# Kernel optimization log

Hardware: AMD Instinct MI355X
Metric: run time of the kernel (lower is better)

Reference implementation:

```python
import jax, jax.numpy as jnp
import numpy as np

SEG = 256  # segment_size from init_kwargs


def setup_inputs() -> dict:
    key = jax.random.key(0)
    ks = jax.random.split(key, 8)
    B, Lq, Lkv, D, H, dk = 2, 1024, 2048, 1024, 16, 64
    s = 1.0 / np.sqrt(D)
    return {
        "q": jax.random.normal(ks[0], (B, Lq, D), jnp.float32),
        "k": jax.random.normal(ks[1], (B, Lkv, D), jnp.float32),
        "v": jax.random.normal(ks[2], (B, Lkv, D), jnp.float32),
        "Wq": jax.random.normal(ks[3], (H, D, dk), jnp.float32) * s,
        "bq": jnp.zeros((H, dk), jnp.float32),
        "Wk": jax.random.normal(ks[4], (H, D, dk), jnp.float32) * s,
        "bk": jnp.zeros((H, dk), jnp.float32),
        "Wv": jax.random.normal(ks[5], (D, dk), jnp.float32) * s,
        "bv": jnp.zeros((dk,), jnp.float32),
        "Wh": jax.random.normal(ks[6], (dk, D), jnp.float32) * s,
    }


def reference(q, k, v, Wq, bq, Wk, bk, Wv, bv, Wh):
    B, Lq, D = q.shape
    kv_len = k.shape[1]
    S = SEG
    nseg = kv_len // S  # kv_len divisible by S -> no padding branch
    H, _, dk = Wq.shape
    dv = Wv.shape[-1]

    kseg = k.reshape(B, nseg, S, D)
    vseg = v.reshape(B, nseg, S, D)

    # per-head linear projections
    qs = jnp.einsum('bqd,hdk->bhqk', q, Wq) + bq[:, None, :]            # [B,H,Lq,dk]
    kp = jnp.einsum('bnsd,hdk->bhnsk', kseg, Wk) + bk[:, None, None, :]  # [B,H,n,S,dk]
    vp = jnp.einsum('bnsd,dv->bnsv', vseg, Wv) + bv                      # [B,n,S,dv]

    scale = jnp.sqrt(jnp.asarray(dk, q.dtype))
    attn = jnp.einsum('bhqk,bhnsk->bhnqs', qs, kp) / scale               # [B,H,n,Lq,S]
    # SAME causal mask applied to every segment (no offset), as in source
    causal = jnp.triu(jnp.ones((Lq, S), bool), k=1)
    attn = jnp.where(causal, jnp.asarray(-1e9, attn.dtype), attn)
    attn = jax.nn.softmax(attn, axis=-1)

    out = jnp.einsum('bhnqs,bnsv->bhnqv', attn, vp)                      # [B,H,n,Lq,dv]

    L = nseg * Lq  # segments concatenated along query dim (segment-major)
    head = out.reshape(B, H, L, dv).transpose(0, 2, 1, 3)                # [B,L,H,dv]
    attn_out = attn.reshape(B, H, L, S).transpose(0, 2, 1, 3)            # [B,L,H,S]

    outputs = head.mean(axis=2) @ Wh                                     # [B,L,D]
    return outputs, attn_out
```

## Files before the change

### kernel.cpp

```cpp
#include <hip/hip_runtime.h>


#define B_ 2
#define LQ 1024
#define LKV 2048
#define D_ 1024
#define H_ 16
#define DK 64
#define SEGW 256
#define NSEG 8
#define LTOT 8192

typedef _Float16 f16;
typedef __attribute__((ext_vector_type(8))) _Float16 f16x8;
typedef __attribute__((ext_vector_type(4))) _Float16 f16x4;
typedef __attribute__((ext_vector_type(4))) float f32x4;

#define MFMA_F16(a, b, c) __builtin_amdgcn_mfma_f32_16x16x32_f16((a), (b), (c), 0, 0, 0)

__global__ __launch_bounds__(256) void prep_kernel(
    const float* __restrict__ Wq, const float* __restrict__ Wk,
    const float* __restrict__ Wv, const float* __restrict__ Wh,
    f16* __restrict__ WqT, f16* __restrict__ WkT, f16* __restrict__ WvT,
    f16* __restrict__ WhT) {
  __shared__ float T[32][33];
  const int bid = blockIdx.x;
  const float* src;
  f16* dst;
  int D, N, d0, n0;
  size_t soff = 0, doff = 0;
  if (bid < 2048) {
    int z = bid >> 6, inner = bid & 63;
    int h = z & 15;
    src = (z < 16) ? Wq : Wk;
    dst = (z < 16) ? WqT : WkT;
    soff = (size_t)h * (1024 * 64);
    doff = (size_t)h * (64 * 1024);
    D = 1024; N = 64;
    d0 = (inner & 31) * 32;
    n0 = (inner >> 5) * 32;
  } else if (bid < 2112) {
    int i = bid - 2048;
    src = Wv; dst = WvT; D = 1024; N = 64;
    d0 = (i & 31) * 32;
    n0 = (i >> 5) * 32;
  } else {
    int i = bid - 2112;
    src = Wh; dst = WhT; D = 64; N = 1024;
    d0 = (i & 1) * 32;
    n0 = (i >> 1) * 32;
  }
  const int c = threadIdx.x & 31, r0 = threadIdx.x >> 5;
#pragma unroll
  for (int i = 0; i < 4; ++i) {
    int r = r0 + i * 8;
    T[r][c] = src[soff + (size_t)(d0 + r) * N + n0 + c];
  }
  __syncthreads();
#pragma unroll
  for (int i = 0; i < 4; ++i) {
    int rr = r0 + i * 8;
    dst[doff + (size_t)(n0 + rr) * D + d0 + c] = (f16)T[c][rr];
  }
}

__device__ __forceinline__ void proj_body(
    const float* __restrict__ A, const f16* __restrict__ WT,
    const float* __restrict__ bias, f16* __restrict__ C, int Mb, int bshift,
    int m0, int c0, char* smem) {
  f16(*Ah)[40] = (f16(*)[40])smem;
  f16(*Bh)[40] = (f16(*)[40])(smem + 20480);
  const int tid = threadIdx.x, lane = tid & 63, w = tid >> 6;
  const int wr = w >> 1, wc = w & 1;
  const int l15 = lane & 15, l4 = lane >> 4;
  const int f4 = tid & 7, row0 = tid >> 3;
  const int u = tid & 3, cb = tid >> 2;

  f32x4 acc[4][4];
#pragma unroll
  for (int i = 0; i < 4; ++i)
#pragma unroll
    for (int j = 0; j < 4; ++j) acc[i][j] = (f32x4)0.f;

  float4 aR[4];
  f16x8 bR[2];

#define PLOAD(k0)                                                              \
  {                                                                            \
    _Pragma("unroll") for (int p = 0; p < 4; ++p) aR[p] =                      \
        *(const float4*)(A + (size_t)(m0 + row0 + p * 32) * 1024 + (k0) +      \
                         f4 * 4);                                              \
    _Pragma("unroll") for (int p = 0; p < 2; ++p) bR[p] =                      \
        *(const f16x8*)(WT + (size_t)(c0 + cb + p * 64) * 1024 + (k0) +        \
                        u * 8);                                                \
  }
#define PSTORE(bi)                                                             \
  {                                                                            \
    _Pragma("unroll") for (int p = 0; p < 4; ++p) {                            \
      f16x4 h4;                                                                \
      h4[0] = (f16)aR[p].x; h4[1] = (f16)aR[p].y;                              \
      h4[2] = (f16)aR[p].z; h4[3] = (f16)aR[p].w;                              \
      *(f16x4*)&Ah[(bi)*128 + row0 + p * 32][f4 * 4] = h4;                     \
    }                                                                          \
    _Pragma("unroll") for (int p = 0; p < 2; ++p)                              \
        *(f16x8*)&Bh[(bi)*128 + cb + p * 64][u * 8] = bR[p];                   \
  }

  PLOAD(0);
  PSTORE(0);
  __syncthreads();

#pragma unroll 2
  for (int k = 0; k < 32; ++k) {
    if (k + 1 < 32) PLOAD((k + 1) * 32);
    const int cbuf = (k & 1) * 128;
    f16x8 ah[4], bh[4];
#pragma unroll
    for (int i = 0; i < 4; ++i) {
      ah[i] = *(const f16x8*)&Ah[cbuf + wr * 64 + i * 16 + l15][l4 * 8];
      bh[i] = *(const f16x8*)&Bh[cbuf + wc * 64 + i * 16 + l15][l4 * 8];
    }
#pragma unroll
    for (int i = 0; i < 4; ++i)
#pragma unroll
      for (int j = 0; j < 4; ++j) acc[i][j] = MFMA_F16(ah[i], bh[j], acc[i][j]);
    if (k + 1 < 32) PSTORE((k + 1) & 1);
    __syncthreads();
  }
#undef PLOAD
#undef PSTORE

  f16(*Cst)[136] = (f16(*)[136])smem;
#pragma unroll
  for (int j = 0; j < 4; ++j) {
    int cl = wc * 64 + j * 16 + l15;
    float bs = bias[c0 + cl];
#pragma unroll
    for (int i = 0; i < 4; ++i)
#pragma unroll
      for (int r = 0; r < 4; ++r)
        Cst[wr * 64 + i * 16 + l4 * 4 + r][cl] = (f16)(acc[i][j][r] + bs);
  }
  __syncthreads();
#pragma unroll
  for (int p = 0; p < 8; ++p) {
    int row = p * 16 + (tid >> 4);
    int col = (tid & 15) * 8;
    f16x8 vv = *(const f16x8*)&Cst[row][col];
    int m = m0 + row, c = c0 + col;
    int bb = m >> bshift, ml = m - (bb << bshift);
    int hidx = c >> 6, dk = c & 63;
    *(f16x8*)(C + ((size_t)(bb * 16 + hidx) * Mb + ml) * 64 + dk) = vv;
  }
}

__device__ __forceinline__ void vproj_body(
    const float* __restrict__ v, const f16* __restrict__ WvT,
    const float* __restrict__ bv, f16* __restrict__ vpTg, int m0, char* smem) {
  f16(*Av)[40] = (f16(*)[40])smem;
  f16(*Bv)[40] = (f16(*)[40])(smem + 10240);
  const int tid = threadIdx.x, lane = tid & 63, w = tid >> 6;
  const int l15 = lane & 15, l4 = lane >> 4;
  const int f4 = tid & 7, row0 = tid >> 3;
  const int u = tid & 3, cb = tid >> 2;

  f32x4 acc[4];
#pragma unroll
  for (int j = 0; j < 4; ++j) acc[j] = (f32x4)0.f;

  float4 aR[2];
  f16x8 bR;

#define VLOAD(k0)                                                              \
  {                                                                            \
    _Pragma("unroll") for (int p = 0; p < 2; ++p) aR[p] =                      \
        *(const float4*)(v + (size_t)(m0 + row0 + p * 32) * 1024 + (k0) +      \
                         f4 * 4);                                              \
    bR = *(const f16x8*)(WvT + (size_t)cb * 1024 + (k0) + u * 8);              \
  }
#define VSTORE(bi)                                                             \
  {                                                                            \
    _Pragma("unroll") for (int p = 0; p < 2; ++p) {                            \
      f16x4 h4;                                                                \
      h4[0] = (f16)aR[p].x; h4[1] = (f16)aR[p].y;                              \
      h4[2] = (f16)aR[p].z; h4[3] = (f16)aR[p].w;                              \
      *(f16x4*)&Av[(bi)*64 + row0 + p * 32][f4 * 4] = h4;                      \
    }                                                                          \
    *(f16x8*)&Bv[(bi)*64 + cb][u * 8] = bR;                                    \
  }

  VLOAD(0);
  VSTORE(0);
  __syncthreads();

#pragma unroll 2
  for (int k = 0; k < 32; ++k) {
    if (k + 1 < 32) VLOAD((k + 1) * 32);
    const int cbuf = (k & 1) * 64;
    f16x8 a8 = *(const f16x8*)&Av[cbuf + w * 16 + l15][l4 * 8];
#pragma unroll
    for (int cf = 0; cf < 4; ++cf) {
      f16x8 b8 = *(const f16x8*)&Bv[cbuf + cf * 16 + l15][l4 * 8];
      acc[cf] = MFMA_F16(a8, b8, acc[cf]);
    }
    if (k + 1 < 32) VSTORE((k + 1) & 1);
    __syncthreads();
  }
#undef VLOAD
#undef VSTORE

  f16(*Vst)[72] = (f16(*)[72])smem;
#pragma unroll
  for (int cf = 0; cf < 4; ++cf) {
    float bvv = bv[cf * 16 + l15];
#pragma unroll
    for (int r = 0; r < 4; ++r)
      Vst[cf * 16 + l15][w * 16 + l4 * 4 + r] = (f16)(acc[cf][r] + bvv);
  }
  __syncthreads();
  const int b = m0 >> 11, rest = m0 & 2047, n = rest >> 8, si0 = rest & 255;
#pragma unroll
  for (int p = 0; p < 2; ++p) {
    int row = p * 32 + (tid >> 3);
    int col = (tid & 7) * 8;
    f16x8 vv = *(const f16x8*)&Vst[row][col];
    *(f16x8*)(vpTg + ((size_t)((b * 8 + n) * 64 + row)) * 256 + si0 + col) = vv;
  }
}

__global__ __launch_bounds__(256) void proj_all_kernel(
    const float* __restrict__ q, const float* __restrict__ k,
    const float* __restrict__ v, const f16* __restrict__ WqT,
    const f16* __restrict__ WkT, const f16* __restrict__ WvT,
    const float* __restrict__ bq, const float* __restrict__ bk,
    const float* __restrict__ bv, f16* __restrict__ qs, f16* __restrict__ kp,
    f16* __restrict__ vpTg) {
  __shared__ __align__(16) char smem[40960];
  const int bid = blockIdx.x;
  if (bid < 128) {
    proj_body(q, WqT, bq, qs, 1024, 10, (bid & 15) * 128, (bid >> 4) * 128, smem);
  } else if (bid < 384) {
    int i = bid - 128;
    proj_body(k, WkT, bk, kp, 2048, 11, (i & 31) * 128, (i >> 5) * 128, smem);
  } else {
    vproj_body(v, WvT, bv, vpTg, (bid - 384) * 64, smem);
  }
}

__global__ __launch_bounds__(256, 2) void fused_attn_kernel(
    const f16* __restrict__ qs, const f16* __restrict__ kp,
    const f16* __restrict__ vpTg, float* __restrict__ attn_out,
    f16* __restrict__ mhp) {
  __shared__ __align__(16) char Kbuf[2][32768];

  const int bid = blockIdx.x;
  const int xcd = bid & 7, sub = bid >> 3;
  const int gg = xcd * 4 + (sub >> 4);
  const int qt = sub & 15;
  const int pair = gg & 15, hgIdx = gg >> 4;
  const int b = pair >> 3, n = pair & 7;
  const int q0 = qt * 64;

  const int tid = threadIdx.x, lane = tid & 63, w = tid >> 6;
  const int l15 = lane & 15, l4 = lane >> 4;

  const int laneoff =
      (lane >> 3) * 128 + (((lane & 7) * 16) ^ ((lane >> 3) << 4));

  f16x8 vfrag[8];
  {
    const f16* vb = vpTg + ((size_t)(pair * 64 + w * 16 + l15)) * 256 + l4 * 8;
#pragma unroll
    for (int kc = 0; kc < 8; ++kc) vfrag[kc] = *(const f16x8*)(vb + kc * 32);
  }

#define STAGE_K(bufIdx, h)                                                      \
  {                                                                             \
    const char* src_ = (const char*)kp +                                        \
        ((size_t)((b * 16 + (h)) * 2048 + n * 256)) * 128;                      \
    char* lds_ = &Kbuf[bufIdx][0];                                              \
    _Pragma("unroll")                                                           \
    for (int j_ = 0; j_ < 8; ++j_) {                                            \
      int ch_ = w * 8 + j_;                                                     \
      __builtin_amdgcn_global_load_lds(                                         \
          (const __attribute__((address_space(1))) unsigned int*)(src_ +        \
              ch_ * 1024 + laneoff),                                            \
          (__attribute__((address_space(3))) unsigned int*)(lds_ + ch_ * 1024), \
          16, 0, 0);                                                            \
    }                                                                           \
  }

#define LOAD_Q(h, a0, a1)                                                       \
  {                                                                             \
    const f16* qp_ = qs +                                                       \
        ((size_t)((b * 16 + (h)) * 1024 + q0 + w * 16 + l15)) * 64 + l4 * 8;    \
    a0 = *(const f16x8*)qp_;                                                    \
    a1 = *(const f16x8*)(qp_ + 32);                                             \
  }

  f16x8 qa0, qa1, qn0, qn1;
  STAGE_K(0, hgIdx * 8);
  LOAD_Q(hgIdx * 8, qa0, qa1);
  qn0 = qa0; qn1 = qa1;

  f32x4 accO[4];
#pragma unroll
  for (int i = 0; i < 4; ++i) accO[i] = (f32x4)0.f;

  asm volatile("s_waitcnt vmcnt(2)" ::: "memory");
  __builtin_amdgcn_s_barrier();

#pragma unroll 1
  for (int hh = 0; hh < 8; ++hh) {
    const int h = hgIdx * 8 + hh;
    const int cur = hh & 1;
    if (hh < 7) {
      STAGE_K(cur ^ 1, h + 1);
      LOAD_Q(h + 1, qn0, qn1);
    }

    f32x4 accS[16];
#pragma unroll
    for (int sf = 0; sf < 16; ++sf) accS[sf] = (f32x4)0.f;
    const char* Kc = &Kbuf[cur][0];
    {
      const int sw = (l15 & 7) << 4;
      __builtin_amdgcn_s_setprio(1);
#pragma unroll
      for (int sf = 0; sf < 16; ++sf) {
        const int rowb = (sf * 16 + l15) * 128;
        f16x8 b0 = *(const f16x8*)(Kc + rowb + ((l4 * 16) ^ sw));
        f16x8 b1 = *(const f16x8*)(Kc + rowb + ((64 + l4 * 16) ^ sw));
        accS[sf] = MFMA_F16(qa0, b0, accS[sf]);
        accS[sf] = MFMA_F16(qa1, b1, accS[sf]);
      }
      __builtin_amdgcn_s_setprio(0);
    }

    float inv[4];
#pragma unroll
    for (int r = 0; r < 4; ++r) {
      const int qg = q0 + w * 16 + l4 * 4 + r;
      float mx = -3.0e38f;
      if (q0 < SEGW) {
#pragma unroll
        for (int sf = 0; sf < 16; ++sf) {
          int s = sf * 16 + l15;
          float vv = accS[sf][r] * 0.125f;
          if (s > qg) vv = -3.0e38f;
          accS[sf][r] = vv;
          mx = fmaxf(mx, vv);
        }
      } else {
#pragma unroll
        for (int sf = 0; sf < 16; ++sf) {
          float vv = accS[sf][r] * 0.125f;
          accS[sf][r] = vv;
          mx = fmaxf(mx, vv);
        }
      }
      mx = fmaxf(mx, __shfl_xor(mx, 1));
      mx = fmaxf(mx, __shfl_xor(mx, 2));
      mx = fmaxf(mx, __shfl_xor(mx, 4));
      mx = fmaxf(mx, __shfl_xor(mx, 8));
      float sum = 0.f;
#pragma unroll
      for (int sf = 0; sf < 16; ++sf) {
        float e = __expf(accS[sf][r] - mx);
        accS[sf][r] = e;
        sum += e;
      }
      sum += __shfl_xor(sum, 1);
      sum += __shfl_xor(sum, 2);
      sum += __shfl_xor(sum, 4);
      sum += __shfl_xor(sum, 8);
      inv[r] = 1.0f / sum;
    }

    asm volatile("s_waitcnt lgkmcnt(0)" ::: "memory");
    __builtin_amdgcn_s_barrier();

    char* Pc = &Kbuf[cur][0];
#pragma unroll
    for (int r = 0; r < 4; ++r) {
      const int q = w * 16 + l4 * 4 + r;
      const int sw = (q & 7) << 4;
      const int rowb = q * 512;
#pragma unroll
      for (int sf = 0; sf < 16; ++sf) {
        int s = sf * 16 + l15;
        *(f16*)(Pc + rowb + ((s * 2) ^ sw)) = (f16)(accS[sf][r] * inv[r]);
      }
    }
    asm volatile("s_waitcnt lgkmcnt(0)" ::: "memory");
    __builtin_amdgcn_s_barrier();

    __builtin_amdgcn_s_setprio(1);
#pragma unroll
    for (int kc = 0; kc < 8; ++kc) {
#pragma unroll
      for (int qb = 0; qb < 4; ++qb) {
        const int q = qb * 16 + l15;
        f16x8 pa = *(const f16x8*)(Pc + q * 512 +
                                   ((kc * 64 + l4 * 16) ^ ((q & 7) << 4)));
        accO[qb] = MFMA_F16(pa, vfrag[kc], accO[qb]);
      }
    }
    __builtin_amdgcn_s_setprio(0);

    {
      const size_t base0 =
          (((size_t)b * LTOT + (size_t)n * LQ + q0) * H_ + h) * SEGW;
#pragma unroll
      for (int it = 0; it < 16; ++it) {
        const int q = w * 16 + it;
        f16x4 p4 =
            *(const f16x4*)(Pc + q * 512 + ((lane * 8) ^ ((q & 7) << 4)));
        f32x4 f;
        f[0] = (float)p4[0]; f[1] = (float)p4[1];
        f[2] = (float)p4[2]; f[3] = (float)p4[3];
        __builtin_nontemporal_store(
            f, (f32x4*)(attn_out + base0 + (size_t)q * (H_ * SEGW) + lane * 4));
      }
    }

    qa0 = qn0; qa1 = qn1;
    asm volatile("s_waitcnt lgkmcnt(0)" ::: "memory");
    asm volatile("s_waitcnt vmcnt(16)" ::: "memory");
    __builtin_amdgcn_s_barrier();
  }

  {
    f16* mp = mhp + ((size_t)hgIdx * 16384 + (size_t)pair * 1024 + q0) * 64 +
              w * 16 + l15;
    const float s16 = 1.0f / 16.0f;
#pragma unroll
    for (int qb = 0; qb < 4; ++qb)
#pragma unroll
      for (int r = 0; r < 4; ++r)
        mp[(size_t)(qb * 16 + l4 * 4 + r) * 64] = (f16)(accO[qb][r] * s16);
  }
#undef STAGE_K
#undef LOAD_Q
}

__global__ __launch_bounds__(256) void final_f16_kernel(
    const f16* __restrict__ mhp, const f16* __restrict__ WhT,
    float* __restrict__ outputs) {
  __shared__ __align__(16) char smemF[33792];
  f16(*Af)[72] = (f16(*)[72])smemF;
  f16(*Bf)[72] = (f16(*)[72])(smemF + 9216);
  const int m0 = blockIdx.x * 64, c0 = blockIdx.y * 128;
  const int tid = threadIdx.x, lane = tid & 63, w = tid >> 6;
  const int l15 = lane & 15, l4 = lane >> 4;
  {
    int u = tid & 7, row0 = tid >> 3;
#pragma unroll
    for (int p = 0; p < 2; ++p) {
      int r = row0 + p * 32;
      size_t mi = (size_t)(m0 + r) * 64 + u * 8;
      f16x8 a0 = *(const f16x8*)(mhp + mi);
      f16x8 a1 = *(const f16x8*)(mhp + (size_t)16384 * 64 + mi);
      *(f16x8*)&Af[r][u * 8] = a0 + a1;
    }
    int cb = tid >> 3;
#pragma unroll
    for (int p = 0; p < 4; ++p) {
      int c = cb + p * 32;
      *(f16x8*)&Bf[c][u * 8] = *(const f16x8*)(WhT + (size_t)(c0 + c) * 64 + u * 8);
    }
  }
  __syncthreads();

  f32x4 acc[8];
#pragma unroll
  for (int cf = 0; cf < 8; ++cf) acc[cf] = (f32x4)0.f;
#pragma unroll
  for (int kc = 0; kc < 2; ++kc) {
    f16x8 a8 = *(const f16x8*)&Af[w * 16 + l15][kc * 32 + l4 * 8];
#pragma unroll
    for (int cf = 0; cf < 8; ++cf) {
      f16x8 b8 = *(const f16x8*)&Bf[cf * 16 + l15][kc * 32 + l4 * 8];
      acc[cf] = MFMA_F16(a8, b8, acc[cf]);
    }
  }
  __syncthreads();

  float(*Cst)[132] = (float(*)[132])smemF;
#pragma unroll
  for (int cf = 0; cf < 8; ++cf)
#pragma unroll
    for (int r = 0; r < 4; ++r)
      Cst[w * 16 + l4 * 4 + r][cf * 16 + l15] = acc[cf][r];
  __syncthreads();
#pragma unroll
  for (int p = 0; p < 8; ++p) {
    int row = p * 8 + (tid >> 5);
    int col = (tid & 31) * 4;
    f32x4 vv = *(const f32x4*)&Cst[row][col];
    __builtin_nontemporal_store(
        vv, (f32x4*)(outputs + (size_t)(m0 + row) * 1024 + c0 + col));
  }
}

extern "C" void kernel_launch(void* const* d_in, const int* in_sizes, int n_in,
                              void* d_out, int out_size, void* d_ws,
                              size_t ws_size, hipStream_t stream) {
  const float* q  = (const float*)d_in[0];
  const float* k  = (const float*)d_in[1];
  const float* v  = (const float*)d_in[2];
  const float* Wq = (const float*)d_in[3];
  const float* bq = (const float*)d_in[4];
  const float* Wk = (const float*)d_in[5];
  const float* bk = (const float*)d_in[6];
  const float* Wv = (const float*)d_in[7];
  const float* bv = (const float*)d_in[8];
  const float* Wh = (const float*)d_in[9];

  float* outputs  = (float*)d_out;
  float* attn_out = (float*)d_out + (size_t)B_ * LTOT * D_;

  char* ws = (char*)d_ws;
  f16* WqT  = (f16*)(ws + 0);
  f16* WkT  = (f16*)(ws + (2u << 20));
  f16* WvT  = (f16*)(ws + (4u << 20));
  f16* WhT  = (f16*)(ws + (4u << 20) + 131072);
  f16* qs   = (f16*)(ws + (4u << 20) + 262144);
  f16* kp   = (f16*)((char*)qs + (4u << 20));
  f16* vpTg = (f16*)((char*)kp + (8u << 20));
  f16* mhp  = (f16*)((char*)vpTg + (1u << 19));

  prep_kernel<<<dim3(2176), 256, 0, stream>>>(Wq, Wk, Wv, Wh, WqT, WkT, WvT, WhT);
  proj_all_kernel<<<dim3(448), 256, 0, stream>>>(q, k, v, WqT, WkT, WvT, bq, bk,
                                                 bv, qs, kp, vpTg);
  fused_attn_kernel<<<dim3(512), 256, 0, stream>>>(qs, kp, vpTg, attn_out, mhp);
  final_f16_kernel<<<dim3(256, 8), 256, 0, stream>>>(mhp, WhT, outputs);
}
```

Measured before the change: 118.2 us.

## Transpose QK^T MFMA operands for lane-local softmax and vectorized P stores

```diff
diff --git a/kernel.cpp b/kernel.cpp
--- a/kernel.cpp
+++ b/kernel.cpp
@@ -24,43 +24,47 @@
     f16* __restrict__ WqT, f16* __restrict__ WkT, f16* __restrict__ WvT,
     f16* __restrict__ WhT) {
   __shared__ float T[32][33];
-  const int bid = blockIdx.x;
-  const float* src;
-  f16* dst;
-  int D, N, d0, n0;
-  size_t soff = 0, doff = 0;
-  if (bid < 2048) {
-    int z = bid >> 6, inner = bid & 63;
-    int h = z & 15;
-    src = (z < 16) ? Wq : Wk;
-    dst = (z < 16) ? WqT : WkT;
-    soff = (size_t)h * (1024 * 64);
-    doff = (size_t)h * (64 * 1024);
-    D = 1024; N = 64;
-    d0 = (inner & 31) * 32;
-    n0 = (inner >> 5) * 32;
-  } else if (bid < 2112) {
-    int i = bid - 2048;
-    src = Wv; dst = WvT; D = 1024; N = 64;
-    d0 = (i & 31) * 32;
-    n0 = (i >> 5) * 32;
-  } else {
-    int i = bid - 2112;
-    src = Wh; dst = WhT; D = 64; N = 1024;
-    d0 = (i & 1) * 32;
-    n0 = (i >> 1) * 32;
-  }
   const int c = threadIdx.x & 31, r0 = threadIdx.x >> 5;
-#pragma unroll
-  for (int i = 0; i < 4; ++i) {
-    int r = r0 + i * 8;
-    T[r][c] = src[soff + (size_t)(d0 + r) * N + n0 + c];
-  }
-  __syncthreads();
-#pragma unroll
-  for (int i = 0; i < 4; ++i) {
-    int rr = r0 + i * 8;
-    dst[doff + (size_t)(n0 + rr) * D + d0 + c] = (f16)T[c][rr];
+#pragma unroll 1
+  for (int t = 0; t < 4; ++t) {
+    const int gidx = blockIdx.x * 4 + t;
+    const float* src;
+    f16* dst;
+    int N, D2, d0, n0;
+    size_t soff = 0, doff = 0;
+    if (gidx < 2048) {
+      int z = gidx >> 6, inner = gidx & 63;
+      int h = z & 15;
+      src = (z < 16) ? Wq : Wk;
+      dst = (z < 16) ? WqT : WkT;
+      soff = (size_t)h * (1024 * 64);
+      doff = (size_t)h * (64 * 1024);
+      N = 64; D2 = 1024;
+      d0 = (inner & 31) * 32;
+      n0 = (inner >> 5) * 32;
+    } else if (gidx < 2112) {
+      int i = gidx - 2048;
+      src = Wv; dst = WvT; N = 64; D2 = 1024;
+      d0 = (i & 31) * 32;
+      n0 = (i >> 5) * 32;
+    } else {
+      int i = gidx - 2112;
+      src = Wh; dst = WhT; N = 1024; D2 = 64;
+      d0 = (i & 1) * 32;
+      n0 = (i >> 1) * 32;
+    }
+#pragma unroll
+    for (int i = 0; i < 4; ++i) {
+      int r = r0 + i * 8;
+      T[r][c] = src[soff + (size_t)(d0 + r) * N + n0 + c];
+    }
+    __syncthreads();
+#pragma unroll
+    for (int i = 0; i < 4; ++i) {
+      int rr = r0 + i * 8;
+      dst[doff + (size_t)(n0 + rr) * D2 + d0 + c] = (f16)T[c][rr];
+    }
+    __syncthreads();
   }
 }
 
@@ -310,6 +314,9 @@
   asm volatile("s_waitcnt vmcnt(2)" ::: "memory");
   __builtin_amdgcn_s_barrier();
 
+  const int ql = w * 16 + l15;
+  const int swq = (ql & 7) << 4;
+
 #pragma unroll 1
   for (int hh = 0; hh < 8; ++hh) {
     const int h = hgIdx * 8 + hh;
@@ -331,66 +338,62 @@
         const int rowb = (sf * 16 + l15) * 128;
         f16x8 b0 = *(const f16x8*)(Kc + rowb + ((l4 * 16) ^ sw));
         f16x8 b1 = *(const f16x8*)(Kc + rowb + ((64 + l4 * 16) ^ sw));
-        accS[sf] = MFMA_F16(qa0, b0, accS[sf]);
-        accS[sf] = MFMA_F16(qa1, b1, accS[sf]);
+        accS[sf] = MFMA_F16(b0, qa0, accS[sf]);
+        accS[sf] = MFMA_F16(b1, qa1, accS[sf]);
       }
       __builtin_amdgcn_s_setprio(0);
     }
 
-    float inv[4];
-#pragma unroll
-    for (int r = 0; r < 4; ++r) {
-      const int qg = q0 + w * 16 + l4 * 4 + r;
-      float mx = -3.0e38f;
-      if (q0 < SEGW) {
-#pragma unroll
-        for (int sf = 0; sf < 16; ++sf) {
-          int s = sf * 16 + l15;
+    float mx = -3.0e38f;
+    if (q0 < SEGW) {
+      const int qg = q0 + ql;
+#pragma unroll
+      for (int sf = 0; sf < 16; ++sf)
+#pragma unroll
+        for (int r = 0; r < 4; ++r) {
+          int s = sf * 16 + l4 * 4 + r;
           float vv = accS[sf][r] * 0.125f;
           if (s > qg) vv = -3.0e38f;
           accS[sf][r] = vv;
           mx = fmaxf(mx, vv);
         }
-      } else {
-#pragma unroll
-        for (int sf = 0; sf < 16; ++sf) {
+    } else {
+#pragma unroll
+      for (int sf = 0; sf < 16; ++sf)
+#pragma unroll
+        for (int r = 0; r < 4; ++r) {
           float vv = accS[sf][r] * 0.125f;
           accS[sf][r] = vv;
           mx = fmaxf(mx, vv);
         }
-      }
-      mx = fmaxf(mx, __shfl_xor(mx, 1));
-      mx = fmaxf(mx, __shfl_xor(mx, 2));
-      mx = fmaxf(mx, __shfl_xor(mx, 4));
-      mx = fmaxf(mx, __shfl_xor(mx, 8));
-      float sum = 0.f;
-#pragma unroll
-      for (int sf = 0; sf < 16; ++sf) {
+    }
+    mx = fmaxf(mx, __shfl_xor(mx, 16));
+    mx = fmaxf(mx, __shfl_xor(mx, 32));
+    float sum = 0.f;
+#pragma unroll
+    for (int sf = 0; sf < 16; ++sf)
+#pragma unroll
+      for (int r = 0; r < 4; ++r) {
         float e = __expf(accS[sf][r] - mx);
         accS[sf][r] = e;
         sum += e;
       }
-      sum += __shfl_xor(sum, 1);
-      sum += __shfl_xor(sum, 2);
-      sum += __shfl_xor(sum, 4);
-      sum += __shfl_xor(sum, 8);
-      inv[r] = 1.0f / sum;
-    }
+    sum += __shfl_xor(sum, 16);
+    sum += __shfl_xor(sum, 32);
+    const float inv = 1.0f / sum;
 
     asm volatile("s_waitcnt lgkmcnt(0)" ::: "memory");
     __builtin_amdgcn_s_barrier();
 
     char* Pc = &Kbuf[cur][0];
 #pragma unroll
-    for (int r = 0; r < 4; ++r) {
-      const int q = w * 16 + l4 * 4 + r;
-      const int sw = (q & 7) << 4;
-      const int rowb = q * 512;
-#pragma unroll
-      for (int sf = 0; sf < 16; ++sf) {
-        int s = sf * 16 + l15;
-        *(f16*)(Pc + rowb + ((s * 2) ^ sw)) = (f16)(accS[sf][r] * inv[r]);
-      }
+    for (int sf = 0; sf < 16; ++sf) {
+      f16x4 p4;
+      p4[0] = (f16)(accS[sf][0] * inv);
+      p4[1] = (f16)(accS[sf][1] * inv);
+      p4[2] = (f16)(accS[sf][2] * inv);
+      p4[3] = (f16)(accS[sf][3] * inv);
+      *(f16x4*)(Pc + ql * 512 + ((sf * 32 + l4 * 8) ^ swq)) = p4;
     }
     asm volatile("s_waitcnt lgkmcnt(0)" ::: "memory");
     __builtin_amdgcn_s_barrier();
@@ -400,9 +403,9 @@
     for (int kc = 0; kc < 8; ++kc) {
 #pragma unroll
       for (int qb = 0; qb < 4; ++qb) {
-        const int q = qb * 16 + l15;
-        f16x8 pa = *(const f16x8*)(Pc + q * 512 +
-                                   ((kc * 64 + l4 * 16) ^ ((q & 7) << 4)));
+        const int qr = qb * 16 + l15;
+        f16x8 pa = *(const f16x8*)(Pc + qr * 512 +
+                                   ((kc * 64 + l4 * 16) ^ ((qr & 7) << 4)));
         accO[qb] = MFMA_F16(pa, vfrag[kc], accO[qb]);
       }
     }
@@ -413,14 +416,14 @@
           (((size_t)b * LTOT + (size_t)n * LQ + q0) * H_ + h) * SEGW;
 #pragma unroll
       for (int it = 0; it < 16; ++it) {
-        const int q = w * 16 + it;
+        const int qr = w * 16 + it;
         f16x4 p4 =
-            *(const f16x4*)(Pc + q * 512 + ((lane * 8) ^ ((q & 7) << 4)));
+            *(const f16x4*)(Pc + qr * 512 + ((lane * 8) ^ ((qr & 7) << 4)));
         f32x4 f;
         f[0] = (float)p4[0]; f[1] = (float)p4[1];
         f[2] = (float)p4[2]; f[3] = (float)p4[3];
         __builtin_nontemporal_store(
-            f, (f32x4*)(attn_out + base0 + (size_t)q * (H_ * SEGW) + lane * 4));
+            f, (f32x4*)(attn_out + base0 + (size_t)qr * (H_ * SEGW) + lane * 4));
       }
     }
 
@@ -530,7 +533,7 @@
   f16* vpTg = (f16*)((char*)kp + (8u << 20));
   f16* mhp  = (f16*)((char*)vpTg + (1u << 19));
 
-  prep_kernel<<<dim3(2176), 256, 0, stream>>>(Wq, Wk, Wv, Wh, WqT, WkT, WvT, WhT);
+  prep_kernel<<<dim3(544), 256, 0, stream>>>(Wq, Wk, Wv, Wh, WqT, WkT, WvT, WhT);
   proj_all_kernel<<<dim3(448), 256, 0, stream>>>(q, k, v, WqT, WkT, WvT, bq, bk,
                                                  bv, qs, kp, vpTg);
   fused_attn_kernel<<<dim3(512), 256, 0, stream>>>(qs, kp, vpTg, attn_out, mhp);
```

Result: faster. 115.1 us (-2.6%).
